# Kernel optimization log

Hardware: AMD Instinct MI355X
Metric: run time of the kernel (lower is better)

## Reference

```python
import jax, jax.numpy as jnp
import numpy as np

NUM_HEADS = 4


def _conv1x1(W, b, x):
    # nn.Conv1d(d_model, d_model, kernel_size=1): pointwise channel mix
    return jnp.einsum('oi,bin->bon', W, x) + b[None, :, None]


def _rot3d_rel_position(desc0, pos, lrf):
    # desc0: [b, d, h, n_pts], pos: [b, n, m, 3], lrf: [b, n, 3, 3] (n == n_pts == m)
    b, d, h, npts = desc0.shape
    m = pos.shape[2]
    # rotate-half: pairs (x0, x1) -> (-x1, x0)
    dh = desc0.reshape(b, d // 2, 2, h, npts)
    desc = jnp.concatenate([-dh[:, :, 1:2], dh[:, :, 0:1]], axis=2).reshape(b, d, h, npts)
    # rotate relative positions into each point's local reference frame
    # torch: einsum('bnxy,bnmy->bnmx', lrf.transpose(2,3), pos) == einsum('bnyx,bnmy->bnmx', lrf, pos)
    posl = jnp.einsum('bnyx,bnmy->bnmx', lrf, pos)
    px, py, pz = posl[..., 0], posl[..., 1], posl[..., 2]
    alpha = jnp.arctan(py / px)
    alpha = jnp.where(px < 0, alpha + np.pi, alpha)
    phi = jnp.arctan(pz / jnp.sqrt(px * px + py * py))
    alpha = jnp.where(jnp.isnan(alpha), 0.0, alpha)
    phi = jnp.where(jnp.isnan(phi), 0.0, phi)
    # F.interpolate(nearest, [m,4]) on [b,n,m,2] duplicates the last axis: [a,a,p,p]
    rot = jnp.stack([alpha, alpha, phi, phi], axis=-1)      # [b,n,m,4]
    rot = jnp.tile(rot, (1, 1, 1, d // 4))                  # [b,n,m,d] (head-independent)
    # 5D rotated value tensor (faithful to original math; head axis broadcast)
    return (jnp.einsum('bdhn,bnmd->bdhnm', desc0, jnp.cos(rot))
            + jnp.einsum('bdhn,bnmd->bdhnm', desc, jnp.sin(rot)))


def setup_inputs() -> dict:
    key = jax.random.key(0)
    ks = jax.random.split(key, 13)
    b, d_model, n, m = 4, 256, 256, 256
    s = 1.0 / np.sqrt(d_model)
    inp = {
        'x': jax.random.normal(ks[0], (b, d_model, n), dtype=jnp.float32),
        'source': jax.random.normal(ks[1], (b, d_model, m), dtype=jnp.float32),
        'x_pos': jax.random.normal(ks[2], (b, n, 3), dtype=jnp.float32),
        'src_pos': jax.random.normal(ks[3], (b, m, 3), dtype=jnp.float32),
        'lrf': jax.random.normal(ks[4], (b, n, 3, 3), dtype=jnp.float32),
        'Wq': jax.random.normal(ks[5], (d_model, d_model), dtype=jnp.float32) * s,
        'bq': jax.random.normal(ks[6], (d_model,), dtype=jnp.float32) * 0.02,
        'Wk': jax.random.normal(ks[7], (d_model, d_model), dtype=jnp.float32) * s,
        'bk': jax.random.normal(ks[8], (d_model,), dtype=jnp.float32) * 0.02,
        'Wv': jax.random.normal(ks[9], (d_model, d_model), dtype=jnp.float32) * s,
        'bv': jax.random.normal(ks[10], (d_model,), dtype=jnp.float32) * 0.02,
        'Wm': jax.random.normal(ks[11], (d_model, d_model), dtype=jnp.float32) * s,
        'bm': jax.random.normal(ks[12], (d_model,), dtype=jnp.float32) * 0.02,
        'k': 32,
    }
    return inp


def reference(x, source, x_pos, src_pos, lrf, Wq, bq, Wk, bk, Wv, bv, Wm, bm, k):
    b, d_model, n = x.shape
    m = source.shape[2]
    h = NUM_HEADS
    dim = d_model // h
    q = _conv1x1(Wq, bq, x).reshape(b, dim, h, n)
    key_ = _conv1x1(Wk, bk, source).reshape(b, dim, h, m)
    val = _conv1x1(Wv, bv, source).reshape(b, dim, h, m)
    # 'self' branch: 3D rotary relative-position encoding of values
    rel = x_pos[:, :, None, :] - src_pos[:, None, :, :]  # [b,n,m,3]
    value5 = _rot3d_rel_position(val, rel, lrf)          # [b,dim,h,n,m]
    # dynamic (top-k sparsified) attention
    scores = jnp.einsum('bdhn,bdhm->bhnm', q, key_) / np.float32(dim) ** 0.5
    vals, idx = jax.lax.top_k(scores, k)                 # over key axis m
    probs = jax.nn.softmax(vals, axis=-1)
    bi = jnp.arange(b)[:, None, None, None]
    hi = jnp.arange(h)[None, :, None, None]
    ni = jnp.arange(n)[None, None, :, None]
    sparse = jnp.zeros_like(scores).at[bi, hi, ni, idx].set(probs)
    # note the deliberate m<->n swap on value5 as in the original einsum
    out = jnp.einsum('bhnm,bdhmn->bdhn', sparse, value5)
    return _conv1x1(Wm, bm, out.reshape(b, d_model, n))
```

## Files before the change

kernel.cpp:

```cpp
#include <hip/hip_runtime.h>
#include <math.h>

#define DM 256
#define NP 256
#define NH 4
#define DH 64

typedef unsigned long long u64;
typedef unsigned int u32;

__global__ __launch_bounds__(256) void qkv_proj_kernel(
    const float* __restrict__ x, const float* __restrict__ src,
    const float* __restrict__ Wq, const float* __restrict__ bq,
    const float* __restrict__ Wk, const float* __restrict__ bk,
    const float* __restrict__ Wv, const float* __restrict__ bv,
    float* __restrict__ Qt, float* __restrict__ Kt, float* __restrict__ Vt)
{
  const int tile = blockIdx.x;
  const int mat  = blockIdx.y;
  const int b    = blockIdx.z;
  const int tc = (tile >> 2) * 64;
  const int tp = (tile & 3) * 64;
  const float* W    = (mat == 0) ? Wq : (mat == 1) ? Wk : Wv;
  const float* bias = (mat == 0) ? bq : (mat == 1) ? bk : bv;
  const float* X    = ((mat == 0) ? x : src) + (size_t)b * DM * NP;
  float* T          = ((mat == 0) ? Qt : (mat == 1) ? Kt : Vt) + (size_t)b * NH * NP * DH;

  __shared__ float Ws[2][32][64];
  __shared__ float Xs[2][32][64];
  const int tid = threadIdx.x;
  const int ty = tid >> 4, tx = tid & 15;
  const int c0 = tid >> 3;
  const int k4 = tid & 7;
  const int pX = tid & 15;
  const int kX = tid >> 4;

  float4 wA, wB, xA, xB;
  #define LOADQKV(K0)                                                          \
    wA = *(const float4*)&W[(size_t)(tc + c0)      * DM + (K0) + k4 * 4];      \
    wB = *(const float4*)&W[(size_t)(tc + c0 + 32) * DM + (K0) + k4 * 4];      \
    xA = *(const float4*)&X[(size_t)((K0) + kX)      * NP + tp + pX * 4];      \
    xB = *(const float4*)&X[(size_t)((K0) + kX + 16) * NP + tp + pX * 4];

  #define STOREQKV(BUF)                                                        \
    Ws[BUF][k4*4+0][c0] = wA.x; Ws[BUF][k4*4+1][c0] = wA.y;                    \
    Ws[BUF][k4*4+2][c0] = wA.z; Ws[BUF][k4*4+3][c0] = wA.w;                    \
    Ws[BUF][k4*4+0][c0+32] = wB.x; Ws[BUF][k4*4+1][c0+32] = wB.y;              \
    Ws[BUF][k4*4+2][c0+32] = wB.z; Ws[BUF][k4*4+3][c0+32] = wB.w;              \
    *(float4*)&Xs[BUF][kX][pX*4]      = xA;                                    \
    *(float4*)&Xs[BUF][kX+16][pX*4]   = xB;

  LOADQKV(0);
  STOREQKV(0);
  __syncthreads();

  float acc[4][4];
  #pragma unroll
  for (int i = 0; i < 4; ++i)
    #pragma unroll
    for (int j = 0; j < 4; ++j) acc[i][j] = 0.f;

  for (int ch = 0; ch < 8; ++ch) {
    const int cur = ch & 1;
    if (ch < 7) { LOADQKV((ch + 1) * 32); }
    #pragma unroll
    for (int kk = 0; kk < 32; ++kk) {
      float4 a = *(const float4*)&Ws[cur][kk][ty * 4];
      float4 xv = *(const float4*)&Xs[cur][kk][tx * 4];
      float av[4] = {a.x, a.y, a.z, a.w};
      float xvv[4] = {xv.x, xv.y, xv.z, xv.w};
      #pragma unroll
      for (int i = 0; i < 4; ++i)
        #pragma unroll
        for (int j = 0; j < 4; ++j) acc[i][j] += av[i] * xvv[j];
    }
    if (ch < 7) {
      STOREQKV(cur ^ 1);
      __syncthreads();
    }
  }

  #pragma unroll
  for (int i = 0; i < 4; ++i) {
    const int c = tc + ty * 4 + i;
    const float bb = bias[c];
    #pragma unroll
    for (int j = 0; j < 4; ++j) {
      const int p = tp + tx * 4 + j;
      T[((size_t)(c & 3) * NP + p) * DH + (c >> 2)] = acc[i][j] + bb;
    }
  }
  #undef LOADQKV
  #undef STOREQKV
}

__global__ __launch_bounds__(256) void score_gemm_kernel(
    const float* __restrict__ Qt, const float* __restrict__ Kt,
    float* __restrict__ scores)
{
  const int tile = blockIdx.x;
  const int bh   = blockIdx.y;
  const int tn = (tile >> 2) * 64;
  const int tm = (tile & 3) * 64;
  const float* Qb = Qt + (size_t)bh * NP * DH;
  const float* Kb = Kt + (size_t)bh * NP * DH;

  __shared__ float Qs[64][68];
  __shared__ float Ks[64][68];
  const int tid = threadIdx.x;

  #pragma unroll
  for (int p = 0; p < 4; ++p) {
    const int u = tid + p * 256;
    const int r = u >> 4;
    const int g = u & 15;
    const float4 qv = *(const float4*)&Qb[(size_t)(tn + r) * DH + g * 4];
    const float4 kv = *(const float4*)&Kb[(size_t)(tm + r) * DH + g * 4];
    Qs[g*4+0][r] = qv.x; Qs[g*4+1][r] = qv.y;
    Qs[g*4+2][r] = qv.z; Qs[g*4+3][r] = qv.w;
    Ks[g*4+0][r] = kv.x; Ks[g*4+1][r] = kv.y;
    Ks[g*4+2][r] = kv.z; Ks[g*4+3][r] = kv.w;
  }
  __syncthreads();

  const int ty = tid >> 4, tx = tid & 15;
  float acc[4][4];
  #pragma unroll
  for (int i = 0; i < 4; ++i)
    #pragma unroll
    for (int j = 0; j < 4; ++j) acc[i][j] = 0.f;

  #pragma unroll 4
  for (int d = 0; d < DH; ++d) {
    const float4 a = *(const float4*)&Qs[d][ty * 4];
    const float4 bv = *(const float4*)&Ks[d][tx * 4];
    const float av[4] = {a.x, a.y, a.z, a.w};
    const float bvv[4] = {bv.x, bv.y, bv.z, bv.w};
    #pragma unroll
    for (int i = 0; i < 4; ++i)
      #pragma unroll
      for (int j = 0; j < 4; ++j) acc[i][j] += av[i] * bvv[j];
  }

  float* srow = scores + ((size_t)bh * NP + tn) * NP + tm;
  #pragma unroll
  for (int i = 0; i < 4; ++i) {
    float4 o4;
    o4.x = acc[i][0] * 0.125f; o4.y = acc[i][1] * 0.125f;
    o4.z = acc[i][2] * 0.125f; o4.w = acc[i][3] * 0.125f;
    *(float4*)&srow[(size_t)(ty * 4 + i) * NP + tx * 4] = o4;
  }
}

__global__ __launch_bounds__(256) void attn_topk_kernel(
    const float* __restrict__ scores, const float* __restrict__ Vt,
    const float* __restrict__ x_pos, const float* __restrict__ src_pos,
    const float* __restrict__ lrf,
    const int* __restrict__ kptr,
    float* __restrict__ O)
{
  const int tid  = threadIdx.x;
  const int wid  = tid >> 6;
  const int lane = tid & 63;
  const int bidx = blockIdx.x;
  const int rb   = (bidx & 7) * 128 + (bidx >> 3);
  const int row  = rb * 4 + wid;
  const int n    = row & (NP - 1);
  const int bh   = row >> 8;
  const int b    = bh >> 2;
  const int h    = bh & 3;

  int kk = *kptr;
  if (kk > 64) kk = 64;
  if (kk < 1) kk = 1;

  __shared__ float  eslot[4][64];
  __shared__ int    msel[4][64];
  __shared__ float4 ang[4][64];
  __shared__ float  otile[4][64];

  const float4 s4 = *(const float4*)&scores[(size_t)row * NP + lane * 4];
  float s[4] = { s4.x, s4.y, s4.z, s4.w };
  u32 u[4], lowv[4];
  #pragma unroll
  for (int r = 0; r < 4; ++r) {
    u32 bb = __float_as_uint(s[r]);
    u[r] = (bb & 0x80000000u) ? ~bb : (bb | 0x80000000u);
    lowv[r] = (u32)(255 - (lane * 4 + r));
  }

  u32 T = 0u;
  #pragma unroll
  for (int bit = 31; bit >= 0; --bit) {
    const u32 cand = T | (1u << bit);
    int c = 0;
    #pragma unroll
    for (int r = 0; r < 4; ++r) c += __popcll(__ballot(u[r] >= cand));
    if (c >= kk) T = cand;
  }
  int c_gt = 0;
  #pragma unroll
  for (int r = 0; r < 4; ++r) c_gt += __popcll(__ballot(u[r] > T));

  u32 Lo = 0u;
  #pragma unroll
  for (int bit = 7; bit >= 0; --bit) {
    const u32 cand = Lo | (1u << bit);
    int c = c_gt;
    #pragma unroll
    for (int r = 0; r < 4; ++r)
      c += __popcll(__ballot((u[r] == T) && (lowv[r] >= cand)));
    if (c >= kk) Lo = cand;
  }

  const float sT = __uint_as_float((T & 0x80000000u) ? (T & 0x7fffffffu) : ~T);
  bool sel[4]; float e[4]; u64 selm[4];
  #pragma unroll
  for (int r = 0; r < 4; ++r) {
    sel[r] = (u[r] > T) || ((u[r] == T) && (lowv[r] >= Lo));
    e[r] = sel[r] ? expf(s[r] - sT) : 0.f;
    selm[r] = __ballot(sel[r]);
  }
  float z = e[0] + e[1] + e[2] + e[3];
  #pragma unroll
  for (int off = 32; off; off >>= 1) z += __shfl_xor(z, off);

  const u64 lt = (1ull << lane) - 1ull;
  int base = 0;
  #pragma unroll
  for (int r = 0; r < 4; ++r) {
    if (sel[r]) {
      const int slot = base + __popcll(selm[r] & lt);
      eslot[wid][slot] = e[r];
      msel[wid][slot]  = lane * 4 + r;
    }
    base += __popcll(selm[r]);
  }

  if (lane < kk) {
    const float ej = eslot[wid][lane];
    const int   mj = msel[wid][lane];
    const float p = ej / z;
    const float* xp = x_pos   + ((size_t)b * NP + mj) * 3;
    const float* sp = src_pos + ((size_t)b * NP + n) * 3;
    const float* L  = lrf     + ((size_t)b * NP + mj) * 9;
    const float r0 = xp[0] - sp[0], r1 = xp[1] - sp[1], r2v = xp[2] - sp[2];
    const float px = L[0]*r0 + L[3]*r1 + L[6]*r2v;
    const float py = L[1]*r0 + L[4]*r1 + L[7]*r2v;
    const float pz = L[2]*r0 + L[5]*r1 + L[8]*r2v;
    const float r2 = px*px + py*py;
    const float inv2 = (r2 > 0.f) ? rsqrtf(r2) : 0.f;
    const float ca = (r2 > 0.f) ? px * inv2 : 1.f;
    const float sa = py * inv2;
    const float r2d = r2 * inv2;
    const float r3 = r2 + pz * pz;
    const float inv3 = (r3 > 0.f) ? rsqrtf(r3) : 0.f;
    const float cph = (r3 > 0.f) ? r2d * inv3 : 1.f;
    const float sph = pz * inv3;
    ang[wid][lane] = make_float4(p * ca, p * sa, p * cph, p * sph);
  }

  const float* vbase = Vt + (size_t)bh * NP * DH;
  const bool useA = ((lane & 3) < 2);
  const bool odd  = (lane & 1);
  const int  ev   = lane & ~1;
  float acc = 0.f;

  int j = 0;
  for (; j + 4 <= kk; j += 4) {
    const int ma = msel[wid][j],   mb = msel[wid][j+1];
    const int mc = msel[wid][j+2], md = msel[wid][j+3];
    const float4 Aa = ang[wid][j],   Ab = ang[wid][j+1];
    const float4 Ac = ang[wid][j+2], Ad = ang[wid][j+3];
    const float2 va = *(const float2*)(vbase + (size_t)ma * DH + ev);
    const float2 vb = *(const float2*)(vbase + (size_t)mb * DH + ev);
    const float2 vc = *(const float2*)(vbase + (size_t)mc * DH + ev);
    const float2 vd = *(const float2*)(vbase + (size_t)md * DH + ev);
    float vm, dsc, pc, ps;
    vm = odd ? va.y : va.x;  dsc = odd ? va.x : -va.y;
    pc = useA ? Aa.x : Aa.z; ps  = useA ? Aa.y : Aa.w;
    acc += vm * pc + dsc * ps;
    vm = odd ? vb.y : vb.x;  dsc = odd ? vb.x : -vb.y;
    pc = useA ? Ab.x : Ab.z; ps  = useA ? Ab.y : Ab.w;
    acc += vm * pc + dsc * ps;
    vm = odd ? vc.y : vc.x;  dsc = odd ? vc.x : -vc.y;
    pc = useA ? Ac.x : Ac.z; ps  = useA ? Ac.y : Ac.w;
    acc += vm * pc + dsc * ps;
    vm = odd ? vd.y : vd.x;  dsc = odd ? vd.x : -vd.y;
    pc = useA ? Ad.x : Ad.z; ps  = useA ? Ad.y : Ad.w;
    acc += vm * pc + dsc * ps;
  }
  for (; j < kk; ++j) {
    const int m = msel[wid][j];
    const float4 A = ang[wid][j];
    const float2 v2 = *(const float2*)(vbase + (size_t)m * DH + ev);
    const float vm  = odd ? v2.y :  v2.x;
    const float dsc = odd ? v2.x : -v2.y;
    acc += vm * (useA ? A.x : A.z) + dsc * (useA ? A.y : A.w);
  }

  otile[wid][lane] = acc;
  __syncthreads();
  if (wid == 0) {
    float4 o4;
    o4.x = otile[0][lane]; o4.y = otile[1][lane];
    o4.z = otile[2][lane]; o4.w = otile[3][lane];
    const int c = (lane << 2) | h;
    const int n0 = (rb * 4) & (NP - 1);
    *(float4*)&O[((size_t)b * DM + c) * NP + n0] = o4;
  }
}

__global__ __launch_bounds__(256) void final_proj_kernel(
    const float* __restrict__ O, const float* __restrict__ Wm,
    const float* __restrict__ bm, float* __restrict__ out)
{
  const int tile = blockIdx.x;
  const int b    = blockIdx.y;
  const int tc = (tile >> 2) * 64;
  const int tp = (tile & 3) * 64;
  const float* X = O + (size_t)b * DM * NP;
  float* Y       = out + (size_t)b * DM * NP;

  __shared__ float Ws[2][32][64];
  __shared__ float Xs[2][32][64];
  const int tid = threadIdx.x;
  const int ty = tid >> 4, tx = tid & 15;
  const int c0 = tid >> 3;
  const int k4 = tid & 7;
  const int pX = tid & 15;
  const int kX = tid >> 4;

  float4 wA, wB, xA, xB;
  #define LOADF(K0)                                                            \
    wA = *(const float4*)&Wm[(size_t)(tc + c0)      * DM + (K0) + k4 * 4];     \
    wB = *(const float4*)&Wm[(size_t)(tc + c0 + 32) * DM + (K0) + k4 * 4];     \
    xA = *(const float4*)&X[(size_t)((K0) + kX)      * NP + tp + pX * 4];      \
    xB = *(const float4*)&X[(size_t)((K0) + kX + 16) * NP + tp + pX * 4];

  #define STOREF(BUF)                                                          \
    Ws[BUF][k4*4+0][c0] = wA.x; Ws[BUF][k4*4+1][c0] = wA.y;                    \
    Ws[BUF][k4*4+2][c0] = wA.z; Ws[BUF][k4*4+3][c0] = wA.w;                    \
    Ws[BUF][k4*4+0][c0+32] = wB.x; Ws[BUF][k4*4+1][c0+32] = wB.y;              \
    Ws[BUF][k4*4+2][c0+32] = wB.z; Ws[BUF][k4*4+3][c0+32] = wB.w;              \
    *(float4*)&Xs[BUF][kX][pX*4]      = xA;                                    \
    *(float4*)&Xs[BUF][kX+16][pX*4]   = xB;

  LOADF(0);
  STOREF(0);
  __syncthreads();

  float acc[4][4];
  #pragma unroll
  for (int i = 0; i < 4; ++i)
    #pragma unroll
    for (int j = 0; j < 4; ++j) acc[i][j] = 0.f;

  for (int ch = 0; ch < 8; ++ch) {
    const int cur = ch & 1;
    if (ch < 7) { LOADF((ch + 1) * 32); }
    #pragma unroll
    for (int kk = 0; kk < 32; ++kk) {
      float4 a = *(const float4*)&Ws[cur][kk][ty * 4];
      float4 xv = *(const float4*)&Xs[cur][kk][tx * 4];
      float av[4] = {a.x, a.y, a.z, a.w};
      float xvv[4] = {xv.x, xv.y, xv.z, xv.w};
      #pragma unroll
      for (int i = 0; i < 4; ++i)
        #pragma unroll
        for (int j = 0; j < 4; ++j) acc[i][j] += av[i] * xvv[j];
    }
    if (ch < 7) {
      STOREF(cur ^ 1);
      __syncthreads();
    }
  }

  #pragma unroll
  for (int i = 0; i < 4; ++i) {
    const int c = tc + ty * 4 + i;
    const float bb = bm[c];
    float4 o4;
    o4.x = acc[i][0] + bb; o4.y = acc[i][1] + bb;
    o4.z = acc[i][2] + bb; o4.w = acc[i][3] + bb;
    *(float4*)&Y[(size_t)c * NP + tp + tx * 4] = o4;
  }
  #undef LOADF
  #undef STOREF
}

extern "C" void kernel_launch(void* const* d_in, const int* in_sizes, int n_in,
                              void* d_out, int out_size, void* d_ws, size_t ws_size,
                              hipStream_t stream)
{
  const float* x       = (const float*)d_in[0];
  const float* source  = (const float*)d_in[1];
  const float* x_pos   = (const float*)d_in[2];
  const float* src_pos = (const float*)d_in[3];
  const float* lrf     = (const float*)d_in[4];
  const float* Wq = (const float*)d_in[5];
  const float* bq = (const float*)d_in[6];
  const float* Wk = (const float*)d_in[7];
  const float* bk = (const float*)d_in[8];
  const float* Wv = (const float*)d_in[9];
  const float* bv = (const float*)d_in[10];
  const float* Wm = (const float*)d_in[11];
  const float* bm = (const float*)d_in[12];
  const int* kptr = (const int*)d_in[13];
  float* out = (float*)d_out;

  float* ws = (float*)d_ws;
  float* Qt = ws;
  float* Kt = Qt + 262144;
  float* Vt = Kt + 262144;
  float* O  = Vt + 262144;
  float* scores = O + 262144;

  qkv_proj_kernel<<<dim3(16, 3, 4), 256, 0, stream>>>(
      x, source, Wq, bq, Wk, bk, Wv, bv, Qt, Kt, Vt);
  score_gemm_kernel<<<dim3(16, 16), 256, 0, stream>>>(
      Qt, Kt, scores);
  attn_topk_kernel<<<dim3(1024), 256, 0, stream>>>(
      scores, Vt, x_pos, src_pos, lrf, kptr, O);
  final_proj_kernel<<<dim3(16, 4), 256, 0, stream>>>(
      O, Wm, bm, out);
}
```

Baseline: 52.46 us.

## Split-K the QKV and output projections and fuse partial reductions downstream

The QKV projection now splits the reduction dimension in two, doubling the block count, and writes raw partial sums in channel-major layout. The score GEMM sums the partials, adds biases, and also builds the transposed V tile. The final projection is split four ways along K, and a new merge kernel sums the partials and adds the bias. The attention gather loop now software-pipelines the V loads one group ahead. The aim is to fill more CUs in small-grid GEMMs, at the cost of extra partial-buffer traffic and one more launch.

```diff
diff --git a/kernel.cpp b/kernel.cpp
--- a/kernel.cpp
+++ b/kernel.cpp
@@ -9,22 +9,22 @@
 typedef unsigned long long u64;
 typedef unsigned int u32;
 
-__global__ __launch_bounds__(256) void qkv_proj_kernel(
+__global__ __launch_bounds__(256) void qkv_part_kernel(
     const float* __restrict__ x, const float* __restrict__ src,
-    const float* __restrict__ Wq, const float* __restrict__ bq,
-    const float* __restrict__ Wk, const float* __restrict__ bk,
-    const float* __restrict__ Wv, const float* __restrict__ bv,
-    float* __restrict__ Qt, float* __restrict__ Kt, float* __restrict__ Vt)
+    const float* __restrict__ Wq, const float* __restrict__ Wk,
+    const float* __restrict__ Wv,
+    float* __restrict__ Ppart)
 {
   const int tile = blockIdx.x;
   const int mat  = blockIdx.y;
-  const int b    = blockIdx.z;
+  const int bz   = blockIdx.z;
+  const int b  = bz >> 1;
+  const int ks = bz & 1;
   const int tc = (tile >> 2) * 64;
   const int tp = (tile & 3) * 64;
-  const float* W    = (mat == 0) ? Wq : (mat == 1) ? Wk : Wv;
-  const float* bias = (mat == 0) ? bq : (mat == 1) ? bk : bv;
-  const float* X    = ((mat == 0) ? x : src) + (size_t)b * DM * NP;
-  float* T          = ((mat == 0) ? Qt : (mat == 1) ? Kt : Vt) + (size_t)b * NH * NP * DH;
+  const float* W = (mat == 0) ? Wq : (mat == 1) ? Wk : Wv;
+  const float* X = ((mat == 0) ? x : src) + (size_t)b * DM * NP;
+  float* P = Ppart + ((size_t)((ks * 3 + mat) * 4 + b)) * 65536;
 
   __shared__ float Ws[2][32][64];
   __shared__ float Xs[2][32][64];
@@ -34,6 +34,7 @@
   const int k4 = tid & 7;
   const int pX = tid & 15;
   const int kX = tid >> 4;
+  const int kbase = ks * 128;
 
   float4 wA, wB, xA, xB;
   #define LOADQKV(K0)                                                          \
@@ -50,7 +51,7 @@
     *(float4*)&Xs[BUF][kX][pX*4]      = xA;                                    \
     *(float4*)&Xs[BUF][kX+16][pX*4]   = xB;
 
-  LOADQKV(0);
+  LOADQKV(kbase);
   STOREQKV(0);
   __syncthreads();
 
@@ -60,9 +61,9 @@
     #pragma unroll
     for (int j = 0; j < 4; ++j) acc[i][j] = 0.f;
 
-  for (int ch = 0; ch < 8; ++ch) {
+  for (int ch = 0; ch < 4; ++ch) {
     const int cur = ch & 1;
-    if (ch < 7) { LOADQKV((ch + 1) * 32); }
+    if (ch < 3) { LOADQKV(kbase + (ch + 1) * 32); }
     #pragma unroll
     for (int kk = 0; kk < 32; ++kk) {
       float4 a = *(const float4*)&Ws[cur][kk][ty * 4];
@@ -74,7 +75,7 @@
         #pragma unroll
         for (int j = 0; j < 4; ++j) acc[i][j] += av[i] * xvv[j];
     }
-    if (ch < 7) {
+    if (ch < 3) {
       STOREQKV(cur ^ 1);
       __syncthreads();
     }
@@ -82,44 +83,57 @@
 
   #pragma unroll
   for (int i = 0; i < 4; ++i) {
-    const int c = tc + ty * 4 + i;
-    const float bb = bias[c];
-    #pragma unroll
-    for (int j = 0; j < 4; ++j) {
-      const int p = tp + tx * 4 + j;
-      T[((size_t)(c & 3) * NP + p) * DH + (c >> 2)] = acc[i][j] + bb;
-    }
+    float4 o4;
+    o4.x = acc[i][0]; o4.y = acc[i][1]; o4.z = acc[i][2]; o4.w = acc[i][3];
+    *(float4*)&P[(size_t)(tc + ty * 4 + i) * NP + tp + tx * 4] = o4;
   }
   #undef LOADQKV
   #undef STOREQKV
 }
 
 __global__ __launch_bounds__(256) void score_gemm_kernel(
-    const float* __restrict__ Qt, const float* __restrict__ Kt,
-    float* __restrict__ scores)
+    const float* __restrict__ Ppart,
+    const float* __restrict__ bq, const float* __restrict__ bk,
+    const float* __restrict__ bv,
+    float* __restrict__ scores, float* __restrict__ Vt)
 {
   const int tile = blockIdx.x;
   const int bh   = blockIdx.y;
   const int tn = (tile >> 2) * 64;
   const int tm = (tile & 3) * 64;
-  const float* Qb = Qt + (size_t)bh * NP * DH;
-  const float* Kb = Kt + (size_t)bh * NP * DH;
+  const int b = bh >> 2, h = bh & 3;
+
+  const float* PQ0 = Ppart + ((size_t)( 0 + b)) * 65536;
+  const float* PQ1 = Ppart + ((size_t)(12 + b)) * 65536;
+  const float* PK0 = Ppart + ((size_t)( 4 + b)) * 65536;
+  const float* PK1 = Ppart + ((size_t)(16 + b)) * 65536;
+  const float* PV0 = Ppart + ((size_t)( 8 + b)) * 65536;
+  const float* PV1 = Ppart + ((size_t)(20 + b)) * 65536;
 
   __shared__ float Qs[64][68];
   __shared__ float Ks[64][68];
+  __shared__ float Vs[16][68];
   const int tid = threadIdx.x;
 
   #pragma unroll
-  for (int p = 0; p < 4; ++p) {
-    const int u = tid + p * 256;
-    const int r = u >> 4;
-    const int g = u & 15;
-    const float4 qv = *(const float4*)&Qb[(size_t)(tn + r) * DH + g * 4];
-    const float4 kv = *(const float4*)&Kb[(size_t)(tm + r) * DH + g * 4];
-    Qs[g*4+0][r] = qv.x; Qs[g*4+1][r] = qv.y;
-    Qs[g*4+2][r] = qv.z; Qs[g*4+3][r] = qv.w;
-    Ks[g*4+0][r] = kv.x; Ks[g*4+1][r] = kv.y;
-    Ks[g*4+2][r] = kv.z; Ks[g*4+3][r] = kv.w;
+  for (int pass = 0; pass < 4; ++pass) {
+    const int u  = tid + pass * 256;
+    const int pg = u & 15;
+    const int d  = u >> 4;
+    const int c  = d * 4 + h;
+    const float bqv = bq[c], bkv = bk[c];
+    const float4 q0 = *(const float4*)&PQ0[(size_t)c * NP + tn + pg * 4];
+    const float4 q1 = *(const float4*)&PQ1[(size_t)c * NP + tn + pg * 4];
+    const float4 k0 = *(const float4*)&PK0[(size_t)c * NP + tm + pg * 4];
+    const float4 k1 = *(const float4*)&PK1[(size_t)c * NP + tm + pg * 4];
+    Qs[d][pg*4+0] = q0.x + q1.x + bqv;
+    Qs[d][pg*4+1] = q0.y + q1.y + bqv;
+    Qs[d][pg*4+2] = q0.z + q1.z + bqv;
+    Qs[d][pg*4+3] = q0.w + q1.w + bqv;
+    Ks[d][pg*4+0] = k0.x + k1.x + bkv;
+    Ks[d][pg*4+1] = k0.y + k1.y + bkv;
+    Ks[d][pg*4+2] = k0.z + k1.z + bkv;
+    Ks[d][pg*4+3] = k0.w + k1.w + bkv;
   }
   __syncthreads();
 
@@ -132,10 +146,10 @@
 
   #pragma unroll 4
   for (int d = 0; d < DH; ++d) {
-    const float4 a = *(const float4*)&Qs[d][ty * 4];
-    const float4 bv = *(const float4*)&Ks[d][tx * 4];
-    const float av[4] = {a.x, a.y, a.z, a.w};
-    const float bvv[4] = {bv.x, bv.y, bv.z, bv.w};
+    const float4 a  = *(const float4*)&Qs[d][ty * 4];
+    const float4 bvv4 = *(const float4*)&Ks[d][tx * 4];
+    const float av[4]  = {a.x, a.y, a.z, a.w};
+    const float bvv[4] = {bvv4.x, bvv4.y, bvv4.z, bvv4.w};
     #pragma unroll
     for (int i = 0; i < 4; ++i)
       #pragma unroll
@@ -149,6 +163,26 @@
     o4.x = acc[i][0] * 0.125f; o4.y = acc[i][1] * 0.125f;
     o4.z = acc[i][2] * 0.125f; o4.w = acc[i][3] * 0.125f;
     *(float4*)&srow[(size_t)(ty * 4 + i) * NP + tx * 4] = o4;
+  }
+
+  {
+    const int dV = tid >> 2;
+    const int mg = tid & 3;
+    const int cV = dV * 4 + h;
+    const float bvb = bv[cV];
+    const float4 v0 = *(const float4*)&PV0[(size_t)cV * NP + tile * 16 + mg * 4];
+    const float4 v1 = *(const float4*)&PV1[(size_t)cV * NP + tile * 16 + mg * 4];
+    Vs[mg*4+0][dV] = v0.x + v1.x + bvb;
+    Vs[mg*4+1][dV] = v0.y + v1.y + bvb;
+    Vs[mg*4+2][dV] = v0.z + v1.z + bvb;
+    Vs[mg*4+3][dV] = v0.w + v1.w + bvb;
+  }
+  __syncthreads();
+  {
+    const int mrow = tid >> 4;
+    const int dg   = tid & 15;
+    const float4 o = *(const float4*)&Vs[mrow][dg * 4];
+    *(float4*)&Vt[((size_t)bh * NP + tile * 16 + mrow) * DH + dg * 4] = o;
   }
 }
 
@@ -266,38 +300,47 @@
   const int  ev   = lane & ~1;
   float acc = 0.f;
 
+  #define ACCSTEP(V2, A4) {                                                   \
+    const float vm  = odd ? (V2).y :  (V2).x;                                 \
+    const float dsc = odd ? (V2).x : -(V2).y;                                 \
+    acc += vm  * (useA ? (A4).x : (A4).z)                                     \
+         + dsc * (useA ? (A4).y : (A4).w); }
+
   int j = 0;
-  for (; j + 4 <= kk; j += 4) {
-    const int ma = msel[wid][j],   mb = msel[wid][j+1];
-    const int mc = msel[wid][j+2], md = msel[wid][j+3];
-    const float4 Aa = ang[wid][j],   Ab = ang[wid][j+1];
-    const float4 Ac = ang[wid][j+2], Ad = ang[wid][j+3];
-    const float2 va = *(const float2*)(vbase + (size_t)ma * DH + ev);
-    const float2 vb = *(const float2*)(vbase + (size_t)mb * DH + ev);
-    const float2 vc = *(const float2*)(vbase + (size_t)mc * DH + ev);
-    const float2 vd = *(const float2*)(vbase + (size_t)md * DH + ev);
-    float vm, dsc, pc, ps;
-    vm = odd ? va.y : va.x;  dsc = odd ? va.x : -va.y;
-    pc = useA ? Aa.x : Aa.z; ps  = useA ? Aa.y : Aa.w;
-    acc += vm * pc + dsc * ps;
-    vm = odd ? vb.y : vb.x;  dsc = odd ? vb.x : -vb.y;
-    pc = useA ? Ab.x : Ab.z; ps  = useA ? Ab.y : Ab.w;
-    acc += vm * pc + dsc * ps;
-    vm = odd ? vc.y : vc.x;  dsc = odd ? vc.x : -vc.y;
-    pc = useA ? Ac.x : Ac.z; ps  = useA ? Ac.y : Ac.w;
-    acc += vm * pc + dsc * ps;
-    vm = odd ? vd.y : vd.x;  dsc = odd ? vd.x : -vd.y;
-    pc = useA ? Ad.x : Ad.z; ps  = useA ? Ad.y : Ad.w;
-    acc += vm * pc + dsc * ps;
+  float2 v0, v1, v2, v3;
+  if (kk >= 4) {
+    const int a0 = msel[wid][0], a1 = msel[wid][1];
+    const int a2 = msel[wid][2], a3 = msel[wid][3];
+    v0 = *(const float2*)(vbase + (size_t)a0 * DH + ev);
+    v1 = *(const float2*)(vbase + (size_t)a1 * DH + ev);
+    v2 = *(const float2*)(vbase + (size_t)a2 * DH + ev);
+    v3 = *(const float2*)(vbase + (size_t)a3 * DH + ev);
+  }
+  for (; j + 8 <= kk; j += 4) {
+    const int n0 = msel[wid][j+4], n1 = msel[wid][j+5];
+    const int n2 = msel[wid][j+6], n3 = msel[wid][j+7];
+    const float2 w0 = *(const float2*)(vbase + (size_t)n0 * DH + ev);
+    const float2 w1 = *(const float2*)(vbase + (size_t)n1 * DH + ev);
+    const float2 w2 = *(const float2*)(vbase + (size_t)n2 * DH + ev);
+    const float2 w3 = *(const float2*)(vbase + (size_t)n3 * DH + ev);
+    const float4 A0 = ang[wid][j],   A1 = ang[wid][j+1];
+    const float4 A2 = ang[wid][j+2], A3 = ang[wid][j+3];
+    ACCSTEP(v0, A0); ACCSTEP(v1, A1); ACCSTEP(v2, A2); ACCSTEP(v3, A3);
+    v0 = w0; v1 = w1; v2 = w2; v3 = w3;
+  }
+  if (j + 4 <= kk) {
+    const float4 A0 = ang[wid][j],   A1 = ang[wid][j+1];
+    const float4 A2 = ang[wid][j+2], A3 = ang[wid][j+3];
+    ACCSTEP(v0, A0); ACCSTEP(v1, A1); ACCSTEP(v2, A2); ACCSTEP(v3, A3);
+    j += 4;
   }
   for (; j < kk; ++j) {
     const int m = msel[wid][j];
-    const float4 A = ang[wid][j];
-    const float2 v2 = *(const float2*)(vbase + (size_t)m * DH + ev);
-    const float vm  = odd ? v2.y :  v2.x;
-    const float dsc = odd ? v2.x : -v2.y;
-    acc += vm * (useA ? A.x : A.z) + dsc * (useA ? A.y : A.w);
-  }
+    const float2 vv = *(const float2*)(vbase + (size_t)m * DH + ev);
+    const float4 A  = ang[wid][j];
+    ACCSTEP(vv, A);
+  }
+  #undef ACCSTEP
 
   otile[wid][lane] = acc;
   __syncthreads();
@@ -311,16 +354,17 @@
   }
 }
 
-__global__ __launch_bounds__(256) void final_proj_kernel(
+__global__ __launch_bounds__(256) void final_part_kernel(
     const float* __restrict__ O, const float* __restrict__ Wm,
-    const float* __restrict__ bm, float* __restrict__ out)
+    float* __restrict__ Pf)
 {
   const int tile = blockIdx.x;
-  const int b    = blockIdx.y;
+  const int ks   = blockIdx.y;
+  const int b    = blockIdx.z;
   const int tc = (tile >> 2) * 64;
   const int tp = (tile & 3) * 64;
   const float* X = O + (size_t)b * DM * NP;
-  float* Y       = out + (size_t)b * DM * NP;
+  float* P = Pf + (size_t)ks * (DM * NP * 4) + (size_t)b * DM * NP;
 
   __shared__ float Ws[2][32][64];
   __shared__ float Xs[2][32][64];
@@ -330,6 +374,7 @@
   const int k4 = tid & 7;
   const int pX = tid & 15;
   const int kX = tid >> 4;
+  const int kbase = ks * 64;
 
   float4 wA, wB, xA, xB;
   #define LOADF(K0)                                                            \
@@ -346,7 +391,7 @@
     *(float4*)&Xs[BUF][kX][pX*4]      = xA;                                    \
     *(float4*)&Xs[BUF][kX+16][pX*4]   = xB;
 
-  LOADF(0);
+  LOADF(kbase);
   STOREF(0);
   __syncthreads();
 
@@ -356,9 +401,9 @@
     #pragma unroll
     for (int j = 0; j < 4; ++j) acc[i][j] = 0.f;
 
-  for (int ch = 0; ch < 8; ++ch) {
+  for (int ch = 0; ch < 2; ++ch) {
     const int cur = ch & 1;
-    if (ch < 7) { LOADF((ch + 1) * 32); }
+    if (ch < 1) { LOADF(kbase + 32); }
     #pragma unroll
     for (int kk = 0; kk < 32; ++kk) {
       float4 a = *(const float4*)&Ws[cur][kk][ty * 4];
@@ -370,7 +415,7 @@
         #pragma unroll
         for (int j = 0; j < 4; ++j) acc[i][j] += av[i] * xvv[j];
     }
-    if (ch < 7) {
+    if (ch < 1) {
       STOREF(cur ^ 1);
       __syncthreads();
     }
@@ -378,15 +423,33 @@
 
   #pragma unroll
   for (int i = 0; i < 4; ++i) {
-    const int c = tc + ty * 4 + i;
-    const float bb = bm[c];
     float4 o4;
-    o4.x = acc[i][0] + bb; o4.y = acc[i][1] + bb;
-    o4.z = acc[i][2] + bb; o4.w = acc[i][3] + bb;
-    *(float4*)&Y[(size_t)c * NP + tp + tx * 4] = o4;
+    o4.x = acc[i][0]; o4.y = acc[i][1]; o4.z = acc[i][2]; o4.w = acc[i][3];
+    *(float4*)&P[(size_t)(tc + ty * 4 + i) * NP + tp + tx * 4] = o4;
   }
   #undef LOADF
   #undef STOREF
+}
+
+__global__ __launch_bounds__(256) void final_merge_kernel(
+    const float* __restrict__ Pf, const float* __restrict__ bm,
+    float* __restrict__ out)
+{
+  const int u = blockIdx.x * 256 + threadIdx.x;
+  const int c = (u >> 6) & 255;
+  const float bb = bm[c];
+  const size_t stride = (size_t)DM * NP * 4 / 4;
+  const float4* P4 = (const float4*)Pf;
+  float4 a = P4[u];
+  float4 b2 = P4[u + stride];
+  float4 c2 = P4[u + 2 * stride];
+  float4 d2 = P4[u + 3 * stride];
+  float4 o;
+  o.x = a.x + b2.x + c2.x + d2.x + bb;
+  o.y = a.y + b2.y + c2.y + d2.y + bb;
+  o.z = a.z + b2.z + c2.z + d2.z + bb;
+  o.w = a.w + b2.w + c2.w + d2.w + bb;
+  ((float4*)out)[u] = o;
 }
 
 extern "C" void kernel_launch(void* const* d_in, const int* in_sizes, int n_in,
@@ -410,18 +473,20 @@
   float* out = (float*)d_out;
 
   float* ws = (float*)d_ws;
-  float* Qt = ws;
-  float* Kt = Qt + 262144;
-  float* Vt = Kt + 262144;
-  float* O  = Vt + 262144;
-  float* scores = O + 262144;
-
-  qkv_proj_kernel<<<dim3(16, 3, 4), 256, 0, stream>>>(
-      x, source, Wq, bq, Wk, bk, Wv, bv, Qt, Kt, Vt);
+  float* Ppart  = ws;
+  float* scores = Ppart + 1572864;
+  float* Vt     = scores + 1048576;
+  float* O      = Vt + 262144;
+  float* Pf     = O + 262144;
+
+  qkv_part_kernel<<<dim3(16, 3, 8), 256, 0, stream>>>(
+      x, source, Wq, Wk, Wv, Ppart);
   score_gemm_kernel<<<dim3(16, 16), 256, 0, stream>>>(
-      Qt, Kt, scores);
+      Ppart, bq, bk, bv, scores, Vt);
   attn_topk_kernel<<<dim3(1024), 256, 0, stream>>>(
       scores, Vt, x_pos, src_pos, lrf, kptr, O);
-  final_proj_kernel<<<dim3(16, 4), 256, 0, stream>>>(
-      O, Wm, bm, out);
-}
+  final_part_kernel<<<dim3(16, 4, 4), 256, 0, stream>>>(
+      O, Wm, Pf);
+  final_merge_kernel<<<dim3(256), 256, 0, stream>>>(
+      Pf, bm, out);
+}
```

After: 43.57 us. 1.2x faster.
